# Kernel tuning notes

Hardware: AMD Instinct MI355X
Metric: run time of the kernel (lower is better)

The kernel has to match this reference:

```python
import jax, jax.numpy as jnp
import numpy as np

SEQ, BATCH = 512, 256
VOCAB = 50000
EMB = 200
HID = 50
MLP = 100


def _run_gru(gx, Whh, bhh, reverse=False):
    # gx: (S, B, 3H) precomputed input-gate activations; PyTorch gate order [r, z, n]
    H = Whh.shape[1]
    B = gx.shape[1]
    h0 = jnp.zeros((B, H), dtype=gx.dtype)

    def step(h, gxt):
        gh = h @ Whh.T + bhh                      # (B, 3H)
        r = jax.nn.sigmoid(gxt[:, :H] + gh[:, :H])
        z = jax.nn.sigmoid(gxt[:, H:2 * H] + gh[:, H:2 * H])
        n = jnp.tanh(gxt[:, 2 * H:] + r * gh[:, 2 * H:])
        h_new = (1.0 - z) * n + z * h
        return h_new, h_new

    _, hs = jax.lax.scan(step, h0, gx, reverse=reverse)
    return hs  # (S, B, H), outputs aligned with input time order


def setup_inputs() -> dict:
    key = jax.random.key(0)
    ks = jax.random.split(key, 12)
    s = 0.1
    inp = {
        "tokens": jax.random.randint(ks[0], (SEQ, BATCH), 0, VOCAB),
        "emb": jax.random.normal(ks[1], (VOCAB + 1, EMB), jnp.float32) * s,
        "Wih_f": jax.random.normal(ks[2], (3 * HID, EMB), jnp.float32) * s,
        "Whh_f": jax.random.normal(ks[3], (3 * HID, HID), jnp.float32) * s,
        "bih_f": jax.random.normal(ks[4], (3 * HID,), jnp.float32) * s,
        "bhh_f": jax.random.normal(ks[5], (3 * HID,), jnp.float32) * s,
        "Wih_b": jax.random.normal(ks[6], (3 * HID, EMB), jnp.float32) * s,
        "Whh_b": jax.random.normal(ks[7], (3 * HID, HID), jnp.float32) * s,
        "bih_b": jax.random.normal(ks[8], (3 * HID,), jnp.float32) * s,
        "bhh_b": jax.random.normal(ks[9], (3 * HID,), jnp.float32) * s,
        "W_mlp": jax.random.normal(ks[10], (MLP, 2 * HID), jnp.float32) * s,
        "b_mlp": jnp.zeros((MLP,), jnp.float32),
        "ctx": jax.random.normal(ks[11], (MLP, 1), jnp.float32) * s,
    }
    return inp


def reference(tokens, emb, Wih_f, Whh_f, bih_f, bhh_f,
              Wih_b, Whh_b, bih_b, bhh_b, W_mlp, b_mlp, ctx):
    e = emb[tokens]                                   # (S, B, E)
    gx_f = e @ Wih_f.T + bih_f                        # (S, B, 3H)
    gx_b = e @ Wih_b.T + bih_b
    h_f = _run_gru(gx_f, Whh_f, bhh_f, reverse=False)
    h_b = _run_gru(gx_b, Whh_b, bhh_b, reverse=True)
    h = jnp.concatenate([h_f, h_b], axis=-1)          # (S, B, 2H)
    u = jnp.tanh(h @ W_mlp.T + b_mlp)                 # (S, B, MLP)
    scores = u @ ctx                                  # (S, B, 1)
    alpha = jax.nn.softmax(scores, axis=0)            # softmax over sequence dim
    # attention-weighted sum over sequence: fused broadcast-multiply-reduce
    doc = jnp.sum(alpha * h, axis=0)                  # (B, 2H)
    return doc
```

## Files before the change

### kernel.cpp

```cpp
#include <hip/hip_runtime.h>
#include <hip/hip_bf16.h>

#define SEQ   512
#define BATCH 256
#define EMB   200
#define HID   50
#define G3    150
#define MLPN  100

typedef __attribute__((ext_vector_type(8))) short bf16x8;
typedef __attribute__((ext_vector_type(4))) float f32x4;

__device__ __forceinline__ unsigned short f2bf(float x) {
    unsigned u = __float_as_uint(x);
    unsigned r = (u + 0x7FFFu + ((u >> 16) & 1u)) >> 16;
    return (unsigned short)r;
}

#define GLOAD_LDS16(g, s) __builtin_amdgcn_global_load_lds( \
    (const __attribute__((address_space(1))) void*)(g),     \
    (__attribute__((address_space(3))) void*)(s), 16, 0, 0)

__global__ __launch_bounds__(256) void k0_wpad(
    const float* __restrict__ Wih_f, const float* __restrict__ Wih_b,
    unsigned short* __restrict__ Wpad)
{
    int idx = blockIdx.x * 256 + threadIdx.x;
    if (idx >= 320 * 224) return;
    int row = idx / 224;
    int k   = idx - row * 224;
    int d   = row / 160;
    int r   = row - d * 160;
    float v = 0.f;
    if (r < G3 && k < EMB) v = (d ? Wih_b : Wih_f)[r * EMB + k];
    Wpad[idx] = f2bf(v);
}

__global__ __launch_bounds__(256) void k1_gx(
    const int* __restrict__ tokens, const float* __restrict__ emb,
    const unsigned short* __restrict__ Wpad,
    const float* __restrict__ bih_f, const float* __restrict__ bih_b,
    float* __restrict__ gx)
{
    __shared__ unsigned short Abuf[64 * 32];
    __shared__ unsigned short Bbuf[320 * 32];
    __shared__ float bias[320];
    __shared__ int tok[64];

    const int t = threadIdx.x;
    const int w = t >> 6;
    const int l = t & 63;
    const long row0 = (long)blockIdx.x * 64;

    for (int idx = t; idx < 320; idx += 256) {
        int d = idx / 160, r = idx - d * 160;
        bias[idx] = (r < G3) ? (d ? bih_b[r] : bih_f[r]) : 0.f;
    }
    if (t < 64) tok[t] = tokens[row0 + t];

    f32x4 acc[20];
    #pragma unroll
    for (int nt = 0; nt < 20; nt++) acc[nt] = (f32x4){0.f, 0.f, 0.f, 0.f};

    const int ar = t >> 2;
    const int kq = t & 3;
    __syncthreads();

    for (int c = 0; c < 7; c++) {
        const int kc0 = c * 32;
        float4 v0 = {0,0,0,0}, v1 = {0,0,0,0};
        if (kc0 + kq * 8 < EMB) {
            const float* src = emb + (long)tok[ar] * EMB + kc0 + kq * 8;
            v0 = *reinterpret_cast<const float4*>(src);
            v1 = *reinterpret_cast<const float4*>(src + 4);
        }
        __syncthreads();
        unsigned p0 = f2bf(v0.x) | ((unsigned)f2bf(v0.y) << 16);
        unsigned p1 = f2bf(v0.z) | ((unsigned)f2bf(v0.w) << 16);
        unsigned p2 = f2bf(v1.x) | ((unsigned)f2bf(v1.y) << 16);
        unsigned p3 = f2bf(v1.z) | ((unsigned)f2bf(v1.w) << 16);
        *reinterpret_cast<uint2*>(&Abuf[ar * 32 + kq * 8])     = make_uint2(p0, p1);
        *reinterpret_cast<uint2*>(&Abuf[ar * 32 + kq * 8 + 4]) = make_uint2(p2, p3);
        #pragma unroll
        for (int q = 0; q < 5; q++) {
            const int rbase = w * 80 + q * 16;
            const int rb = rbase + (l >> 2);
            const unsigned short* gsrc = Wpad + (long)rb * 224 + kc0 + (l & 3) * 8;
            GLOAD_LDS16(gsrc, &Bbuf[rbase * 32]);
        }
        __syncthreads();
        bf16x8 af = *reinterpret_cast<bf16x8*>(&Abuf[(w * 16 + (l & 15)) * 32 + (l >> 4) * 8]);
        #pragma unroll
        for (int nt = 0; nt < 20; nt++) {
            bf16x8 bfr = *reinterpret_cast<bf16x8*>(&Bbuf[(nt * 16 + (l & 15)) * 32 + (l >> 4) * 8]);
            acc[nt] = __builtin_amdgcn_mfma_f32_16x16x32_bf16(af, bfr, acc[nt], 0, 0, 0);
        }
    }

    const int colL  = l & 15;
    const int rquad = l >> 4;
    #pragma unroll
    for (int nt = 0; nt < 20; nt++) {
        int pcol = nt * 16 + colL;
        int d = pcol / 160;
        int jc = pcol - d * 160;
        if (jc >= G3) continue;
        float bv = bias[pcol];
        long col = d * G3 + jc;
        #pragma unroll
        for (int i = 0; i < 4; i++) {
            long row = row0 + w * 16 + rquad * 4 + i;
            gx[row * 300 + col] = acc[nt][i] + bv;
        }
    }
}

__global__ __launch_bounds__(192) void k2_gru(
    const float* __restrict__ gx,
    const float* __restrict__ Whh_f, const float* __restrict__ bhh_f,
    const float* __restrict__ Whh_b, const float* __restrict__ bhh_b,
    float* __restrict__ h)
{
    const int b   = blockIdx.x & 255;
    const int dir = blockIdx.x >> 8;
    const float* Whh = dir ? Whh_b : Whh_f;
    const float* bhh = dir ? bhh_b : bhh_f;
    const int j = threadIdx.x;

    __shared__ float hs[HID];
    __shared__ float ghs[G3];
    __shared__ float gxs[G3];

    float w[HID];
    float bj = 0.f;
    if (j < G3) {
        bj = bhh[j];
        #pragma unroll
        for (int k = 0; k < HID; k++) w[k] = Whh[j * HID + k];
    }
    if (j < HID) hs[j] = 0.f;
    float hold = 0.f;
    __syncthreads();

    for (int s = 0; s < SEQ; s++) {
        const int t = dir ? (SEQ - 1 - s) : s;
        float acc = bj;
        if (j < G3) {
            float gxv = gx[((long)t * BATCH + b) * 300 + dir * G3 + j];
            #pragma unroll
            for (int k = 0; k < HID; k++) acc += w[k] * hs[k];
            ghs[j] = acc;
            gxs[j] = gxv;
        }
        __syncthreads();
        if (j < HID) {
            float ghr = ghs[j], ghz = ghs[j + HID], ghn = ghs[j + 2 * HID];
            float gxr = gxs[j], gxz = gxs[j + HID], gxn = gxs[j + 2 * HID];
            float r = 1.f / (1.f + __expf(-(gxr + ghr)));
            float z = 1.f / (1.f + __expf(-(gxz + ghz)));
            float x = gxn + r * ghn;
            float e2 = __expf(-2.f * x);
            float n = (1.f - e2) / (1.f + e2);
            float hn = (1.f - z) * n + z * hold;
            hold = hn;
            hs[j] = hn;
            h[((long)t * BATCH + b) * 100 + dir * HID + j] = hn;
        }
        __syncthreads();
    }
}

__global__ __launch_bounds__(256) void k3_scores(
    const float* __restrict__ h, const float* __restrict__ W_mlp,
    const float* __restrict__ b_mlp, const float* __restrict__ ctx,
    float* __restrict__ scT)
{
    __shared__ float4 Wm[MLPN * 25];
    __shared__ float bm[MLPN], cx[MLPN];
    const int tid = threadIdx.x;
    for (int idx = tid; idx < MLPN * 25; idx += 256)
        Wm[idx] = reinterpret_cast<const float4*>(W_mlp)[idx];
    if (tid < MLPN) { bm[tid] = b_mlp[tid]; cx[tid] = ctx[tid]; }
    __syncthreads();

    const long row = (long)blockIdx.x * 256 + tid;
    float4 hr[25];
    const float4* hp = reinterpret_cast<const float4*>(h + row * 100);
    #pragma unroll
    for (int i = 0; i < 25; i++) hr[i] = hp[i];

    float s = 0.f;
    for (int jj = 0; jj < MLPN; jj++) {
        float acc = bm[jj];
        #pragma unroll
        for (int i = 0; i < 25; i++) {
            float4 wv = Wm[jj * 25 + i];
            acc += wv.x * hr[i].x + wv.y * hr[i].y + wv.z * hr[i].z + wv.w * hr[i].w;
        }
        float e2 = __expf(-2.f * acc);
        float u = (1.f - e2) / (1.f + e2);
        s += u * cx[jj];
    }
    const int t = (int)(row >> 8);
    const int b = (int)(row & 255);
    scT[(long)b * SEQ + t] = s;
}

__global__ __launch_bounds__(128) void k4_doc(
    const float* __restrict__ h, const float* __restrict__ scT,
    float* __restrict__ out)
{
    const int b = blockIdx.x;
    const int tid = threadIdx.x;
    __shared__ float al[SEQ];
    __shared__ float red[128];

    float4 sv = reinterpret_cast<const float4*>(scT + (long)b * SEQ)[tid];
    float m = fmaxf(fmaxf(sv.x, sv.y), fmaxf(sv.z, sv.w));
    red[tid] = m;
    __syncthreads();
    if (tid < 64) red[tid] = fmaxf(red[tid], red[tid + 64]);
    __syncthreads();
    if (tid < 64) {
        float v = red[tid];
        for (int o = 32; o > 0; o >>= 1) v = fmaxf(v, __shfl_down(v, o));
        if (tid == 0) red[0] = v;
    }
    __syncthreads();
    m = red[0];
    float e0 = __expf(sv.x - m), e1 = __expf(sv.y - m);
    float e2 = __expf(sv.z - m), e3 = __expf(sv.w - m);
    float psum = e0 + e1 + e2 + e3;
    __syncthreads();
    red[tid] = psum;
    __syncthreads();
    if (tid < 64) red[tid] += red[tid + 64];
    __syncthreads();
    if (tid < 64) {
        float v = red[tid];
        for (int o = 32; o > 0; o >>= 1) v += __shfl_down(v, o);
        if (tid == 0) red[0] = v;
    }
    __syncthreads();
    const float inv = 1.f / red[0];
    al[tid * 4 + 0] = e0 * inv;
    al[tid * 4 + 1] = e1 * inv;
    al[tid * 4 + 2] = e2 * inv;
    al[tid * 4 + 3] = e3 * inv;
    __syncthreads();

    if (tid < MLPN) {
        float acc = 0.f;
        for (int t = 0; t < SEQ; t++)
            acc += al[t] * h[((long)t * BATCH + b) * 100 + tid];
        out[(long)b * 100 + tid] = acc;
    }
}

extern "C" void kernel_launch(void* const* d_in, const int* in_sizes, int n_in,
                              void* d_out, int out_size, void* d_ws, size_t ws_size,
                              hipStream_t stream)
{
    const int*   tokens = (const int*)d_in[0];
    const float* emb    = (const float*)d_in[1];
    const float* Wih_f  = (const float*)d_in[2];
    const float* Whh_f  = (const float*)d_in[3];
    const float* bih_f  = (const float*)d_in[4];
    const float* bhh_f  = (const float*)d_in[5];
    const float* Wih_b  = (const float*)d_in[6];
    const float* Whh_b  = (const float*)d_in[7];
    const float* bih_b  = (const float*)d_in[8];
    const float* bhh_b  = (const float*)d_in[9];
    const float* W_mlp  = (const float*)d_in[10];
    const float* b_mlp  = (const float*)d_in[11];
    const float* ctx    = (const float*)d_in[12];
    float* out = (float*)d_out;

    float* gx  = (float*)d_ws;
    float* h   = gx + (size_t)SEQ * BATCH * 300;
    float* scT = h  + (size_t)SEQ * BATCH * 100;
    unsigned short* Wpad = (unsigned short*)scT;

    k0_wpad<<<280, 256, 0, stream>>>(Wih_f, Wih_b, Wpad);
    k1_gx<<<2048, 256, 0, stream>>>(tokens, emb, Wpad, bih_f, bih_b, gx);
    k2_gru<<<512, 192, 0, stream>>>(gx, Whh_f, bhh_f, Whh_b, bhh_b, h);
    k3_scores<<<512, 256, 0, stream>>>(h, W_mlp, b_mlp, ctx, scT);
    k4_doc<<<256, 128, 0, stream>>>(h, scT, out);
}
```

Before: 602.0 us.

## Run GRU recurrence in a single wavefront with no barriers and prefetched gates

Restructures the GRU kernel so one 64-lane wavefront handles each (batch, direction) pair. Each lane computes all three gate dot products for one hidden unit, reading h from LDS as float4. This removes both per-step __syncthreads and the staging of gate results through shared memory. Input-gate values are also prefetched two timesteps ahead to hide global load latency. The cost is higher register pressure from 156 weights per lane, 14 idle lanes, and correctness that depends on lanes within a wavefront running in lockstep.

```diff
diff --git a/kernel.cpp b/kernel.cpp
--- a/kernel.cpp
+++ b/kernel.cpp
@@ -115,7 +115,48 @@
     }
 }
 
-__global__ __launch_bounds__(192) void k2_gru(
+#define K2_LOAD(S, VR, VZ, VN) do {                                        \
+    int t_ = dir ? (SEQ - 1 - (S)) : (S);                                  \
+    const float* p_ = gx + (long)t_ * (BATCH * 300) + base;                \
+    VR = p_[0]; VZ = p_[50]; VN = p_[100];                                 \
+} while (0)
+
+#define K2_STEP(S, VR, VZ, VN) do {                                        \
+    int t_ = dir ? (SEQ - 1 - (S)) : (S);                                  \
+    float gxr_ = VR, gxz_ = VZ, gxn_ = VN;                                 \
+    if ((S) + 2 < SEQ) K2_LOAD((S) + 2, VR, VZ, VN);                       \
+    float4 h4_[13];                                                        \
+    _Pragma("unroll")                                                      \
+    for (int i_ = 0; i_ < 13; i_++)                                        \
+        h4_[i_] = reinterpret_cast<float4*>(hs)[i_];                       \
+    float ar_ = br, az_ = bz, an_ = bn;                                    \
+    _Pragma("unroll")                                                      \
+    for (int i_ = 0; i_ < 13; i_++) {                                      \
+        ar_ = fmaf(wr[4*i_],   h4_[i_].x, ar_);                            \
+        az_ = fmaf(wz[4*i_],   h4_[i_].x, az_);                            \
+        an_ = fmaf(wn[4*i_],   h4_[i_].x, an_);                            \
+        ar_ = fmaf(wr[4*i_+1], h4_[i_].y, ar_);                            \
+        az_ = fmaf(wz[4*i_+1], h4_[i_].y, az_);                            \
+        an_ = fmaf(wn[4*i_+1], h4_[i_].y, an_);                            \
+        ar_ = fmaf(wr[4*i_+2], h4_[i_].z, ar_);                            \
+        az_ = fmaf(wz[4*i_+2], h4_[i_].z, az_);                            \
+        an_ = fmaf(wn[4*i_+2], h4_[i_].z, an_);                            \
+        ar_ = fmaf(wr[4*i_+3], h4_[i_].w, ar_);                            \
+        az_ = fmaf(wz[4*i_+3], h4_[i_].w, az_);                            \
+        an_ = fmaf(wn[4*i_+3], h4_[i_].w, an_);                            \
+    }                                                                      \
+    float r_ = 1.f / (1.f + __expf(-(gxr_ + ar_)));                        \
+    float z_ = 1.f / (1.f + __expf(-(gxz_ + az_)));                        \
+    float x_ = gxn_ + r_ * an_;                                            \
+    float e2_ = __expf(-2.f * x_);                                         \
+    float n_ = (1.f - e2_) / (1.f + e2_);                                  \
+    float hn_ = (1.f - z_) * n_ + z_ * hold;                               \
+    hold = hn_;                                                            \
+    h[((long)t_ * BATCH + b) * 100 + dir * 50 + l] = hn_;                  \
+    hs[l] = hn_;                                                           \
+} while (0)
+
+__global__ __launch_bounds__(64) void k2_gru(
     const float* __restrict__ gx,
     const float* __restrict__ Whh_f, const float* __restrict__ bhh_f,
     const float* __restrict__ Whh_b, const float* __restrict__ bhh_b,
@@ -123,50 +164,38 @@
 {
     const int b   = blockIdx.x & 255;
     const int dir = blockIdx.x >> 8;
-    const float* Whh = dir ? Whh_b : Whh_f;
-    const float* bhh = dir ? bhh_b : bhh_f;
-    const int j = threadIdx.x;
-
-    __shared__ float hs[HID];
-    __shared__ float ghs[G3];
-    __shared__ float gxs[G3];
-
-    float w[HID];
-    float bj = 0.f;
-    if (j < G3) {
-        bj = bhh[j];
-        #pragma unroll
-        for (int k = 0; k < HID; k++) w[k] = Whh[j * HID + k];
-    }
-    if (j < HID) hs[j] = 0.f;
-    float hold = 0.f;
-    __syncthreads();
-
-    for (int s = 0; s < SEQ; s++) {
-        const int t = dir ? (SEQ - 1 - s) : s;
-        float acc = bj;
-        if (j < G3) {
-            float gxv = gx[((long)t * BATCH + b) * 300 + dir * G3 + j];
-            #pragma unroll
-            for (int k = 0; k < HID; k++) acc += w[k] * hs[k];
-            ghs[j] = acc;
-            gxs[j] = gxv;
-        }
-        __syncthreads();
-        if (j < HID) {
-            float ghr = ghs[j], ghz = ghs[j + HID], ghn = ghs[j + 2 * HID];
-            float gxr = gxs[j], gxz = gxs[j + HID], gxn = gxs[j + 2 * HID];
-            float r = 1.f / (1.f + __expf(-(gxr + ghr)));
-            float z = 1.f / (1.f + __expf(-(gxz + ghz)));
-            float x = gxn + r * ghn;
-            float e2 = __expf(-2.f * x);
-            float n = (1.f - e2) / (1.f + e2);
-            float hn = (1.f - z) * n + z * hold;
-            hold = hn;
-            hs[j] = hn;
-            h[((long)t * BATCH + b) * 100 + dir * HID + j] = hn;
-        }
-        __syncthreads();
+    const float* __restrict__ Whh = dir ? Whh_b : Whh_f;
+    const float* __restrict__ bhh = dir ? bhh_b : bhh_f;
+    const int l = threadIdx.x;
+
+    __shared__ alignas(16) float hs[52];
+
+    float wr[52], wz[52], wn[52];
+    float br = 0.f, bz = 0.f, bn = 0.f;
+
+    if (l < 2) { hs[50 + l] = 0.f; }
+
+    if (l < 50) {
+        hs[l] = 0.f;
+        br = bhh[l]; bz = bhh[l + 50]; bn = bhh[l + 100];
+        #pragma unroll
+        for (int k = 0; k < 50; k++) {
+            wr[k] = Whh[l * HID + k];
+            wz[k] = Whh[(l + 50) * HID + k];
+            wn[k] = Whh[(l + 100) * HID + k];
+        }
+        wr[50] = wr[51] = wz[50] = wz[51] = wn[50] = wn[51] = 0.f;
+
+        const long base = (long)b * 300 + dir * G3 + l;
+        float hold = 0.f;
+        float p0r, p0z, p0n, p1r, p1z, p1n;
+        K2_LOAD(0, p0r, p0z, p0n);
+        K2_LOAD(1, p1r, p1z, p1n);
+
+        for (int s = 0; s < SEQ; s += 2) {
+            K2_STEP(s,     p0r, p0z, p0n);
+            K2_STEP(s + 1, p1r, p1z, p1n);
+        }
     }
 }
 
@@ -283,7 +312,7 @@
 
     k0_wpad<<<280, 256, 0, stream>>>(Wih_f, Wih_b, Wpad);
     k1_gx<<<2048, 256, 0, stream>>>(tokens, emb, Wpad, bih_f, bih_b, gx);
-    k2_gru<<<512, 192, 0, stream>>>(gx, Whh_f, bhh_f, Whh_b, bhh_b, h);
+    k2_gru<<<512, 64, 0, stream>>>(gx, Whh_f, bhh_f, Whh_b, bhh_b, h);
     k3_scores<<<512, 256, 0, stream>>>(h, W_mlp, b_mlp, ctx, scT);
     k4_doc<<<256, 128, 0, stream>>>(h, scT, out);
 }
```

New measurement: 485.7 us. -19.3%, faster.
